# Optimization experiments

Measured on AMD Instinct MI355X. Metric: run time of the kernel, lower is better.

The kernel has to match this reference:

```python
import jax, jax.numpy as jnp
import numpy as np
import math

N_NODES = 100000
N_PAIRS = 640000
F_TOTAL = 128
N_HEADS = 8
HEAD_DIM = F_TOTAL // N_HEADS  # 16


def setup_inputs() -> dict:
    key = jax.random.key(0)
    ks = jax.random.split(key, 8)
    x = jax.random.normal(ks[0], (N_NODES, F_TOTAL), dtype=jnp.float32)
    w_ij = jax.random.normal(ks[1], (N_PAIRS, F_TOTAL), dtype=jnp.float32)
    idx_i = jax.random.randint(ks[2], (N_PAIRS,), 0, N_NODES, dtype=jnp.int32)
    idx_j = jax.random.randint(ks[3], (N_PAIRS,), 0, N_NODES, dtype=jnp.int32)
    phi_r_cut = jax.random.uniform(ks[4], (N_PAIRS,), dtype=jnp.float32)
    # per-head linear weights, nn.Linear convention: y = x @ W.T, W: (out, in)
    s = 1.0 / math.sqrt(HEAD_DIM)
    wq = jax.random.uniform(ks[5], (N_HEADS, HEAD_DIM, HEAD_DIM), jnp.float32, -s, s)
    wk = jax.random.uniform(ks[6], (N_HEADS, HEAD_DIM, HEAD_DIM), jnp.float32, -s, s)
    wv = jax.random.uniform(ks[7], (N_HEADS, HEAD_DIM, HEAD_DIM), jnp.float32, -s, s)
    return {"x": x, "w_ij": w_ij, "idx_i": idx_i, "idx_j": idx_j,
            "phi_r_cut": phi_r_cut, "wq": wq, "wk": wk, "wv": wv}


def reference(x, w_ij, idx_i, idx_j, phi_r_cut, wq, wk, wv):
    n, f = x.shape
    h, d = wq.shape[0], wq.shape[1]
    # split into heads: (H, n, d) and (H, P, d)
    xh = x.reshape(n, h, d).transpose(1, 0, 2)
    wh = w_ij.reshape(-1, h, d).transpose(1, 0, 2)
    # per-head linear projections (y = x @ W.T)
    q = jnp.einsum('hnd,hed->hne', xh, wq)  # (H, n, d)
    k = jnp.einsum('hnd,hed->hne', xh, wk)
    v = jnp.einsum('hnd,hed->hne', xh, wv)
    # filter-modulated dot-product attention coefficients per pair
    alpha = (q[:, idx_i] * wh * k[:, idx_j]).sum(-1) / math.sqrt(d)  # (H, P)
    alpha = alpha * phi_r_cut[None, :]
    # message + scatter-add aggregation
    msg = alpha[..., None] * v[:, idx_j]  # (H, P, d)
    y = jax.vmap(lambda m: jax.ops.segment_sum(m, idx_i, num_segments=n))(msg)  # (H, n, d)
    return y.transpose(1, 0, 2).reshape(n, f)
```

## Files before the change

### kernel.cpp

```cpp
#include <hip/hip_runtime.h>
#include <hip/hip_bf16.h>

#define F_TOTAL 128
#define N_HEADS 8
#define HEAD_DIM 16
#define SCAN_ITEMS 1024

__global__ __launch_bounds__(256) void proj_kernel(
    const float* __restrict__ x,
    const float* __restrict__ wq,
    const float* __restrict__ wk,
    const float* __restrict__ wv,
    float* __restrict__ q, float* __restrict__ k, float* __restrict__ v,
    int n_nodes)
{
    const int gid = blockIdx.x * 256 + threadIdx.x;
    const int f = gid & (F_TOTAL - 1);

    float rq[16], rk[16], rv[16];
    const float4* wq4 = (const float4*)wq;
    const float4* wk4 = (const float4*)wk;
    const float4* wv4 = (const float4*)wv;
    #pragma unroll
    for (int d4 = 0; d4 < 4; ++d4) {
        float4 a = wq4[f * 4 + d4];
        rq[d4*4+0]=a.x; rq[d4*4+1]=a.y; rq[d4*4+2]=a.z; rq[d4*4+3]=a.w;
        float4 b = wk4[f * 4 + d4];
        rk[d4*4+0]=b.x; rk[d4*4+1]=b.y; rk[d4*4+2]=b.z; rk[d4*4+3]=b.w;
        float4 c = wv4[f * 4 + d4];
        rv[d4*4+0]=c.x; rv[d4*4+1]=c.y; rv[d4*4+2]=c.z; rv[d4*4+3]=c.w;
    }
    const int lanebase = (f & 112) & 63;

    const int total = n_nodes * F_TOTAL;
    const int stride = gridDim.x * 256;
    for (int idx = gid; idx < total; idx += stride) {
        const float xval = __builtin_nontemporal_load(x + idx);
        float aq = 0.f, ak = 0.f, av = 0.f;
        #pragma unroll
        for (int d = 0; d < 16; ++d) {
            const float xv = __shfl(xval, lanebase + d);
            aq += xv * rq[d];
            ak += xv * rk[d];
            av += xv * rv[d];
        }
        q[idx] = aq; k[idx] = ak; v[idx] = av;
    }
}

__global__ __launch_bounds__(256) void hist_kernel(
    const int* __restrict__ idx_i, int* __restrict__ hist, int n_pairs)
{
    const int p = blockIdx.x * 256 + threadIdx.x;
    if (p < n_pairs) atomicAdd(&hist[idx_i[p]], 1);
}

__global__ __launch_bounds__(256) void scan_reduce_kernel(
    const int* __restrict__ hist, int* __restrict__ blockSums, int n)
{
    __shared__ int ls[256];
    const int t = threadIdx.x;
    const int base = blockIdx.x * SCAN_ITEMS + t * 4;
    int s = 0;
    if (base + 3 < n) {
        int4 h = *(const int4*)(hist + base);
        s = h.x + h.y + h.z + h.w;
    } else {
        for (int kk = 0; kk < 4; ++kk)
            if (base + kk < n) s += hist[base + kk];
    }
    ls[t] = s;
    __syncthreads();
    for (int off = 128; off > 0; off >>= 1) {
        if (t < off) ls[t] += ls[t + off];
        __syncthreads();
    }
    if (t == 0) blockSums[blockIdx.x] = ls[0];
}

__global__ __launch_bounds__(128) void scan_spine_kernel(
    int* __restrict__ blockSums, int nblk)
{
    __shared__ int ls[128];
    const int t = threadIdx.x;
    const int val = (t < nblk) ? blockSums[t] : 0;
    ls[t] = val;
    __syncthreads();
    for (int off = 1; off < 128; off <<= 1) {
        int add = (t >= off) ? ls[t - off] : 0;
        __syncthreads();
        ls[t] += add;
        __syncthreads();
    }
    if (t < nblk) blockSums[t] = ls[t] - val;
}

__global__ __launch_bounds__(256) void scan_apply_kernel(
    const int* __restrict__ hist, const int* __restrict__ blockSums,
    int* __restrict__ offsets, int n)
{
    __shared__ int ls[256];
    const int t = threadIdx.x;
    const int base = blockIdx.x * SCAN_ITEMS + t * 4;
    int h0 = 0, h1 = 0, h2 = 0, h3 = 0;
    if (base + 3 < n) {
        int4 h = *(const int4*)(hist + base);
        h0 = h.x; h1 = h.y; h2 = h.z; h3 = h.w;
    } else {
        if (base + 0 < n) h0 = hist[base + 0];
        if (base + 1 < n) h1 = hist[base + 1];
        if (base + 2 < n) h2 = hist[base + 2];
        if (base + 3 < n) h3 = hist[base + 3];
    }
    const int tsum = h0 + h1 + h2 + h3;
    ls[t] = tsum;
    __syncthreads();
    for (int off = 1; off < 256; off <<= 1) {
        int add = (t >= off) ? ls[t - off] : 0;
        __syncthreads();
        ls[t] += add;
        __syncthreads();
    }
    int off = blockSums[blockIdx.x] + (ls[t] - tsum);
    if (base + 0 < n) offsets[base + 0] = off; off += h0;
    if (base + 1 < n) offsets[base + 1] = off; off += h1;
    if (base + 2 < n) offsets[base + 2] = off; off += h2;
    if (base + 3 < n) offsets[base + 3] = off;
}

__global__ __launch_bounds__(256) void scatter_kernel(
    const int* __restrict__ idx_i, const int* __restrict__ idx_j,
    const float* __restrict__ phi, const int* __restrict__ offsets,
    int* __restrict__ cursor,
    int* __restrict__ p_s, int* __restrict__ j_s, float* __restrict__ phi_s,
    int n_pairs)
{
    const int p = blockIdx.x * 256 + threadIdx.x;
    if (p < n_pairs) {
        const int i = idx_i[p];
        const int pos = offsets[i] + atomicAdd(&cursor[i], 1);
        p_s[pos]   = p;
        j_s[pos]   = idx_j[p];
        phi_s[pos] = phi[p];
    }
}

__global__ __launch_bounds__(256) void segment_kernel(
    const float* __restrict__ q,
    const float* __restrict__ k,
    const float* __restrict__ v,
    const float* __restrict__ w_ij,
    const int* __restrict__ hist,
    const int* __restrict__ offsets,
    const int* __restrict__ p_s,
    const int* __restrict__ j_s,
    const float* __restrict__ phi_s,
    float* __restrict__ out,
    int n_nodes)
{
    const int node = blockIdx.x * 2 + (threadIdx.x >> 7);
    const int f = threadIdx.x & (F_TOTAL - 1);
    if (node >= n_nodes) return;

    const int cnt = hist[node];
    const int start = offsets[node];
    const float qv = q[(size_t)node * F_TOTAL + f];

    float acc = 0.f;
    int c = 0;
    for (; c + 4 <= cnt; c += 4) {
        const int b = start + c;
        const int p0 = p_s[b+0], p1 = p_s[b+1], p2 = p_s[b+2], p3 = p_s[b+3];
        const int j0 = j_s[b+0], j1 = j_s[b+1], j2 = j_s[b+2], j3 = j_s[b+3];
        const float ph0 = phi_s[b+0], ph1 = phi_s[b+1],
                    ph2 = phi_s[b+2], ph3 = phi_s[b+3];

        const float w0 = __builtin_nontemporal_load(w_ij + (size_t)p0 * F_TOTAL + f);
        const float w1 = __builtin_nontemporal_load(w_ij + (size_t)p1 * F_TOTAL + f);
        const float w2 = __builtin_nontemporal_load(w_ij + (size_t)p2 * F_TOTAL + f);
        const float w3 = __builtin_nontemporal_load(w_ij + (size_t)p3 * F_TOTAL + f);
        const float k0 = k[(size_t)j0 * F_TOTAL + f];
        const float k1 = k[(size_t)j1 * F_TOTAL + f];
        const float k2 = k[(size_t)j2 * F_TOTAL + f];
        const float k3 = k[(size_t)j3 * F_TOTAL + f];
        const float v0 = v[(size_t)j0 * F_TOTAL + f];
        const float v1 = v[(size_t)j1 * F_TOTAL + f];
        const float v2 = v[(size_t)j2 * F_TOTAL + f];
        const float v3 = v[(size_t)j3 * F_TOTAL + f];

        float t0 = qv * w0 * k0;
        float t1 = qv * w1 * k1;
        float t2 = qv * w2 * k2;
        float t3 = qv * w3 * k3;
        #pragma unroll
        for (int m = 1; m < 16; m <<= 1) {
            t0 += __shfl_xor(t0, m);
            t1 += __shfl_xor(t1, m);
            t2 += __shfl_xor(t2, m);
            t3 += __shfl_xor(t3, m);
        }
        acc += t0 * 0.25f * ph0 * v0;
        acc += t1 * 0.25f * ph1 * v1;
        acc += t2 * 0.25f * ph2 * v2;
        acc += t3 * 0.25f * ph3 * v3;
    }
    for (; c < cnt; ++c) {
        const int b = start + c;
        const int p = p_s[b];
        const int j = j_s[b];
        const float ph = phi_s[b];
        const float wv = __builtin_nontemporal_load(w_ij + (size_t)p * F_TOTAL + f);
        const float kv = k[(size_t)j * F_TOTAL + f];
        const float vv = v[(size_t)j * F_TOTAL + f];
        float t = qv * wv * kv;
        #pragma unroll
        for (int m = 1; m < 16; m <<= 1) t += __shfl_xor(t, m);
        acc += t * 0.25f * ph * vv;
    }
    __builtin_nontemporal_store(acc, out + (size_t)node * F_TOTAL + f);
}

extern "C" void kernel_launch(void* const* d_in, const int* in_sizes, int n_in,
                              void* d_out, int out_size, void* d_ws, size_t ws_size,
                              hipStream_t stream)
{
    const float* x     = (const float*)d_in[0];
    const float* w_ij  = (const float*)d_in[1];
    const int*   idx_i = (const int*)d_in[2];
    const int*   idx_j = (const int*)d_in[3];
    const float* phi   = (const float*)d_in[4];
    const float* wq    = (const float*)d_in[5];
    const float* wk    = (const float*)d_in[6];
    const float* wv    = (const float*)d_in[7];

    const int n_nodes = in_sizes[0] / F_TOTAL;
    const int n_pairs = in_sizes[2];
    const size_t node_elems = (size_t)n_nodes * F_TOTAL;

    float* q         = (float*)d_ws;
    float* k         = q + node_elems;
    float* v         = k + node_elems;
    int*   hist      = (int*)(v + node_elems);
    int*   cursor    = hist + n_nodes;
    int*   offsets   = cursor + n_nodes;
    int*   blockSums = offsets + n_nodes;
    int*   p_s       = blockSums + 128;
    int*   j_s       = p_s + n_pairs;
    float* phi_s     = (float*)(j_s + n_pairs);

    hipMemsetAsync(hist, 0, (size_t)2 * n_nodes * sizeof(int), stream);

    proj_kernel<<<3072, 256, 0, stream>>>(x, wq, wk, wv, q, k, v, n_nodes);

    const int pair_blocks = (n_pairs + 255) / 256;
    hist_kernel<<<pair_blocks, 256, 0, stream>>>(idx_i, hist, n_pairs);

    const int nblk = (n_nodes + SCAN_ITEMS - 1) / SCAN_ITEMS;
    scan_reduce_kernel<<<nblk, 256, 0, stream>>>(hist, blockSums, n_nodes);
    scan_spine_kernel<<<1, 128, 0, stream>>>(blockSums, nblk);
    scan_apply_kernel<<<nblk, 256, 0, stream>>>(hist, blockSums, offsets, n_nodes);

    scatter_kernel<<<pair_blocks, 256, 0, stream>>>(
        idx_i, idx_j, phi, offsets, cursor, p_s, j_s, phi_s, n_pairs);

    segment_kernel<<<(n_nodes + 1) / 2, 256, 0, stream>>>(
        q, k, v, w_ij, hist, offsets, p_s, j_s, phi_s, (float*)d_out, n_nodes);
}
```

Before: 693.7 us.

## Interleave K/V, pack pair metadata, vectorize segment kernel, fuse histogram into projection

Measured after the change: 632.4 us. -8.8%, faster.

```diff
diff --git a/kernel.cpp b/kernel.cpp
--- a/kernel.cpp
+++ b/kernel.cpp
@@ -1,20 +1,26 @@
 #include <hip/hip_runtime.h>
-#include <hip/hip_bf16.h>
 
 #define F_TOTAL 128
 #define N_HEADS 8
 #define HEAD_DIM 16
 #define SCAN_ITEMS 1024
 
-__global__ __launch_bounds__(256) void proj_kernel(
+typedef float vf4 __attribute__((ext_vector_type(4)));
+typedef int   vi4 __attribute__((ext_vector_type(4)));
+typedef float vf2 __attribute__((ext_vector_type(2)));
+
+__global__ __launch_bounds__(256) void proj_hist_kernel(
     const float* __restrict__ x,
     const float* __restrict__ wq,
     const float* __restrict__ wk,
     const float* __restrict__ wv,
-    float* __restrict__ q, float* __restrict__ k, float* __restrict__ v,
-    int n_nodes)
+    const int*   __restrict__ idx_i,
+    float* __restrict__ q, float* __restrict__ kv,
+    int*   __restrict__ hist,
+    int n_nodes, int n_pairs)
 {
     const int gid = blockIdx.x * 256 + threadIdx.x;
+    const int stride = gridDim.x * 256;
     const int f = gid & (F_TOTAL - 1);
 
     float rq[16], rk[16], rv[16];
@@ -33,7 +39,6 @@
     const int lanebase = (f & 112) & 63;
 
     const int total = n_nodes * F_TOTAL;
-    const int stride = gridDim.x * 256;
     for (int idx = gid; idx < total; idx += stride) {
         const float xval = __builtin_nontemporal_load(x + idx);
         float aq = 0.f, ak = 0.f, av = 0.f;
@@ -44,15 +49,12 @@
             ak += xv * rk[d];
             av += xv * rv[d];
         }
-        q[idx] = aq; k[idx] = ak; v[idx] = av;
-    }
-}
-
-__global__ __launch_bounds__(256) void hist_kernel(
-    const int* __restrict__ idx_i, int* __restrict__ hist, int n_pairs)
-{
-    const int p = blockIdx.x * 256 + threadIdx.x;
-    if (p < n_pairs) atomicAdd(&hist[idx_i[p]], 1);
+        q[idx] = aq;
+        ((vf2*)kv)[idx] = (vf2){ak, av};
+    }
+
+    for (int p = gid; p < n_pairs; p += stride)
+        atomicAdd(&hist[idx_i[p]], 1);
 }
 
 __global__ __launch_bounds__(256) void scan_reduce_kernel(
@@ -130,94 +132,76 @@
 
 __global__ __launch_bounds__(256) void scatter_kernel(
     const int* __restrict__ idx_i, const int* __restrict__ idx_j,
-    const float* __restrict__ phi, const int* __restrict__ offsets,
-    int* __restrict__ cursor,
-    int* __restrict__ p_s, int* __restrict__ j_s, float* __restrict__ phi_s,
+    const float* __restrict__ phi,
+    int* __restrict__ offsets,
+    vi4* __restrict__ meta,
     int n_pairs)
 {
     const int p = blockIdx.x * 256 + threadIdx.x;
     if (p < n_pairs) {
         const int i = idx_i[p];
-        const int pos = offsets[i] + atomicAdd(&cursor[i], 1);
-        p_s[pos]   = p;
-        j_s[pos]   = idx_j[p];
-        phi_s[pos] = phi[p];
+        const int pos = atomicAdd(&offsets[i], 1);
+        meta[pos] = (vi4){p, idx_j[p], __float_as_int(phi[p]), 0};
     }
 }
 
 __global__ __launch_bounds__(256) void segment_kernel(
     const float* __restrict__ q,
-    const float* __restrict__ k,
-    const float* __restrict__ v,
+    const float* __restrict__ kv,
     const float* __restrict__ w_ij,
     const int* __restrict__ hist,
     const int* __restrict__ offsets,
-    const int* __restrict__ p_s,
-    const int* __restrict__ j_s,
-    const float* __restrict__ phi_s,
+    const vi4* __restrict__ meta,
     float* __restrict__ out,
     int n_nodes)
 {
-    const int node = blockIdx.x * 2 + (threadIdx.x >> 7);
-    const int f = threadIdx.x & (F_TOTAL - 1);
+    const int node = blockIdx.x * 8 + (threadIdx.x >> 5);
+    const int t = threadIdx.x & 31;
     if (node >= n_nodes) return;
 
     const int cnt = hist[node];
-    const int start = offsets[node];
-    const float qv = q[(size_t)node * F_TOTAL + f];
-
-    float acc = 0.f;
+    const int start = offsets[node] - cnt;
+
+    const vf4 q4 = *((const vf4*)(q + (size_t)node * F_TOTAL) + t);
+    vf4 acc = (vf4){0.f, 0.f, 0.f, 0.f};
+
     int c = 0;
-    for (; c + 4 <= cnt; c += 4) {
-        const int b = start + c;
-        const int p0 = p_s[b+0], p1 = p_s[b+1], p2 = p_s[b+2], p3 = p_s[b+3];
-        const int j0 = j_s[b+0], j1 = j_s[b+1], j2 = j_s[b+2], j3 = j_s[b+3];
-        const float ph0 = phi_s[b+0], ph1 = phi_s[b+1],
-                    ph2 = phi_s[b+2], ph3 = phi_s[b+3];
-
-        const float w0 = __builtin_nontemporal_load(w_ij + (size_t)p0 * F_TOTAL + f);
-        const float w1 = __builtin_nontemporal_load(w_ij + (size_t)p1 * F_TOTAL + f);
-        const float w2 = __builtin_nontemporal_load(w_ij + (size_t)p2 * F_TOTAL + f);
-        const float w3 = __builtin_nontemporal_load(w_ij + (size_t)p3 * F_TOTAL + f);
-        const float k0 = k[(size_t)j0 * F_TOTAL + f];
-        const float k1 = k[(size_t)j1 * F_TOTAL + f];
-        const float k2 = k[(size_t)j2 * F_TOTAL + f];
-        const float k3 = k[(size_t)j3 * F_TOTAL + f];
-        const float v0 = v[(size_t)j0 * F_TOTAL + f];
-        const float v1 = v[(size_t)j1 * F_TOTAL + f];
-        const float v2 = v[(size_t)j2 * F_TOTAL + f];
-        const float v3 = v[(size_t)j3 * F_TOTAL + f];
-
-        float t0 = qv * w0 * k0;
-        float t1 = qv * w1 * k1;
-        float t2 = qv * w2 * k2;
-        float t3 = qv * w3 * k3;
-        #pragma unroll
-        for (int m = 1; m < 16; m <<= 1) {
-            t0 += __shfl_xor(t0, m);
-            t1 += __shfl_xor(t1, m);
-            t2 += __shfl_xor(t2, m);
-            t3 += __shfl_xor(t3, m);
-        }
-        acc += t0 * 0.25f * ph0 * v0;
-        acc += t1 * 0.25f * ph1 * v1;
-        acc += t2 * 0.25f * ph2 * v2;
-        acc += t3 * 0.25f * ph3 * v3;
+    for (; c + 2 <= cnt; c += 2) {
+        const vi4 m0 = meta[start + c];
+        const vi4 m1 = meta[start + c + 1];
+        const vf4 w0 = __builtin_nontemporal_load(
+            (const vf4*)(w_ij + (size_t)m0.x * F_TOTAL) + t);
+        const vf4 w1 = __builtin_nontemporal_load(
+            (const vf4*)(w_ij + (size_t)m1.x * F_TOTAL) + t);
+        const vf4* kp0 = (const vf4*)(kv + (size_t)m0.y * F_TOTAL * 2) + t * 2;
+        const vf4* kp1 = (const vf4*)(kv + (size_t)m1.y * F_TOTAL * 2) + t * 2;
+        const vf4 a0 = kp0[0], b0 = kp0[1];
+        const vf4 a1 = kp1[0], b1 = kp1[1];
+
+        float t0 = q4.x*w0.x*a0.x + q4.y*w0.y*a0.z + q4.z*w0.z*b0.x + q4.w*w0.w*b0.z;
+        float t1 = q4.x*w1.x*a1.x + q4.y*w1.y*a1.z + q4.z*w1.z*b1.x + q4.w*w1.w*b1.z;
+        t0 += __shfl_xor(t0, 1); t0 += __shfl_xor(t0, 2);
+        t1 += __shfl_xor(t1, 1); t1 += __shfl_xor(t1, 2);
+        const float al0 = t0 * 0.25f * __int_as_float(m0.z);
+        const float al1 = t1 * 0.25f * __int_as_float(m1.z);
+        acc.x += al0 * a0.y; acc.y += al0 * a0.w;
+        acc.z += al0 * b0.y; acc.w += al0 * b0.w;
+        acc.x += al1 * a1.y; acc.y += al1 * a1.w;
+        acc.z += al1 * b1.y; acc.w += al1 * b1.w;
     }
     for (; c < cnt; ++c) {
-        const int b = start + c;
-        const int p = p_s[b];
-        const int j = j_s[b];
-        const float ph = phi_s[b];
-        const float wv = __builtin_nontemporal_load(w_ij + (size_t)p * F_TOTAL + f);
-        const float kv = k[(size_t)j * F_TOTAL + f];
-        const float vv = v[(size_t)j * F_TOTAL + f];
-        float t = qv * wv * kv;
-        #pragma unroll
-        for (int m = 1; m < 16; m <<= 1) t += __shfl_xor(t, m);
-        acc += t * 0.25f * ph * vv;
-    }
-    __builtin_nontemporal_store(acc, out + (size_t)node * F_TOTAL + f);
+        const vi4 m0 = meta[start + c];
+        const vf4 w0 = __builtin_nontemporal_load(
+            (const vf4*)(w_ij + (size_t)m0.x * F_TOTAL) + t);
+        const vf4* kp0 = (const vf4*)(kv + (size_t)m0.y * F_TOTAL * 2) + t * 2;
+        const vf4 a0 = kp0[0], b0 = kp0[1];
+        float t0 = q4.x*w0.x*a0.x + q4.y*w0.y*a0.z + q4.z*w0.z*b0.x + q4.w*w0.w*b0.z;
+        t0 += __shfl_xor(t0, 1); t0 += __shfl_xor(t0, 2);
+        const float al0 = t0 * 0.25f * __int_as_float(m0.z);
+        acc.x += al0 * a0.y; acc.y += al0 * a0.w;
+        acc.z += al0 * b0.y; acc.w += al0 * b0.w;
+    }
+    __builtin_nontemporal_store(acc, (vf4*)(out + (size_t)node * F_TOTAL) + t);
 }
 
 extern "C" void kernel_launch(void* const* d_in, const int* in_sizes, int n_in,
@@ -238,31 +222,26 @@
     const size_t node_elems = (size_t)n_nodes * F_TOTAL;
 
     float* q         = (float*)d_ws;
-    float* k         = q + node_elems;
-    float* v         = k + node_elems;
-    int*   hist      = (int*)(v + node_elems);
-    int*   cursor    = hist + n_nodes;
-    int*   offsets   = cursor + n_nodes;
+    float* kv        = q + node_elems;
+    vi4*   meta      = (vi4*)(kv + 2 * node_elems);
+    int*   hist      = (int*)(meta + n_pairs);
+    int*   offsets   = hist + n_nodes;
     int*   blockSums = offsets + n_nodes;
-    int*   p_s       = blockSums + 128;
-    int*   j_s       = p_s + n_pairs;
-    float* phi_s     = (float*)(j_s + n_pairs);
-
-    hipMemsetAsync(hist, 0, (size_t)2 * n_nodes * sizeof(int), stream);
-
-    proj_kernel<<<3072, 256, 0, stream>>>(x, wq, wk, wv, q, k, v, n_nodes);
-
-    const int pair_blocks = (n_pairs + 255) / 256;
-    hist_kernel<<<pair_blocks, 256, 0, stream>>>(idx_i, hist, n_pairs);
+
+    hipMemsetAsync(hist, 0, (size_t)n_nodes * sizeof(int), stream);
+
+    proj_hist_kernel<<<3072, 256, 0, stream>>>(
+        x, wq, wk, wv, idx_i, q, kv, hist, n_nodes, n_pairs);
 
     const int nblk = (n_nodes + SCAN_ITEMS - 1) / SCAN_ITEMS;
     scan_reduce_kernel<<<nblk, 256, 0, stream>>>(hist, blockSums, n_nodes);
     scan_spine_kernel<<<1, 128, 0, stream>>>(blockSums, nblk);
     scan_apply_kernel<<<nblk, 256, 0, stream>>>(hist, blockSums, offsets, n_nodes);
 
+    const int pair_blocks = (n_pairs + 255) / 256;
     scatter_kernel<<<pair_blocks, 256, 0, stream>>>(
-        idx_i, idx_j, phi, offsets, cursor, p_s, j_s, phi_s, n_pairs);
-
-    segment_kernel<<<(n_nodes + 1) / 2, 256, 0, stream>>>(
-        q, k, v, w_ij, hist, offsets, p_s, j_s, phi_s, (float*)d_out, n_nodes);
-}
+        idx_i, idx_j, phi, offsets, meta, n_pairs);
+
+    segment_kernel<<<(n_nodes + 7) / 8, 256, 0, stream>>>(
+        q, kv, w_ij, hist, offsets, meta, (float*)d_out, n_nodes);
+}
```
